# Kernel optimization log

Measured on AMD Instinct MI355X. Metric: run time of the kernel, lower is better.

## Reference

```python
import jax, jax.numpy as jnp
import numpy as np

NEG = -1e9


def setup_inputs() -> dict:
    key = jax.random.key(0)
    ks = jax.random.split(key, 9)
    B, L, S, E = 8, 2048, 2048, 1024
    H, G, KD, VD = 16, 64, 1024, 1024
    return {
        "query": jax.random.normal(ks[0], (B, L, E), jnp.float32),
        "key": jax.random.normal(ks[1], (B, S, E), jnp.float32),
        "value": jax.random.normal(ks[2], (B, S, E), jnp.float32),
        "other": jnp.zeros((1,), jnp.float32),
        "key_padding_mask": jax.random.bernoulli(ks[3], 0.1, (B, S)),
        "nhead": H,
        "query_proj": jax.random.normal(ks[4], (1, E, KD), jnp.float32) * 0.02,
        "key_proj": jax.random.normal(ks[5], (1, E, KD), jnp.float32) * 0.02,
        "value_proj": jax.random.normal(ks[6], (1, E, VD), jnp.float32) * 0.02,
        "importance_proj": jax.random.normal(ks[7], (1, E, H * G), jnp.float32) * 0.02,
        "output_proj": jax.random.normal(ks[8], (1, VD, E), jnp.float32) * 0.02,
    }


def reference(query, key, value, other, key_padding_mask, nhead,
              query_proj, key_proj, value_proj, importance_proj, output_proj):
    B, L, E = query.shape
    S = key.shape[1]
    H = nhead
    KD = query_proj.shape[-1]
    VD = value_proj.shape[-1]
    Ek, Ev = KD // H, VD // H
    G = importance_proj.shape[-1] // H
    scale = 1.0 / jnp.sqrt(jnp.asarray(Ek, query.dtype))

    # projections -> (B, H, L/S, d)
    qs = (query @ query_proj[0]).reshape(B, L, H, Ek).transpose(0, 2, 1, 3)
    kk = (key @ key_proj[0]).reshape(B, S, H, Ek).transpose(0, 2, 1, 3)
    vs = (value @ value_proj[0]).reshape(B, S, H, Ev).transpose(0, 2, 1, 3)

    # importance-weighted global queries: softmax over L
    ips = (query @ importance_proj[0]).reshape(B, L, H, G).transpose(0, 2, 3, 1)  # (B,H,G,L)
    ips = jax.nn.softmax(ips, axis=-1)
    gqs = jnp.einsum('bhgl,bhld->bhgd', ips, qs)  # (B,H,G,Ek)

    # stage 1: global queries attend over all keys (shared attn for keys & values)
    g_scores = jnp.einsum('bhgd,bhsd->bhgs', gqs, kk) * scale  # (B,H,G,S)
    g_scores = jnp.where(key_padding_mask[:, None, None, :], NEG, g_scores)
    g_attn = jax.nn.softmax(g_scores, axis=-1)
    global_keys = jnp.einsum('bhgs,bhsd->bhgd', g_attn, kk)   # (B,H,G,Ek)
    global_values = jnp.einsum('bhgs,bhsd->bhgd', g_attn, vs)  # (B,H,G,Ev)

    # stage 2: local queries attend over G global keys/values
    l_scores = jnp.einsum('bhld,bhgd->bhlg', qs, global_keys) * scale  # (B,H,L,G)
    l_attn = jax.nn.softmax(l_scores, axis=-1)
    out = jnp.einsum('bhlg,bhgd->bhld', l_attn, global_values)  # (B,H,L,Ev)

    out = out.transpose(0, 2, 1, 3).reshape(B, L, H * Ev)
    out = out @ output_proj[0]  # (B,L,E)
    return (out, l_attn)
```

## Files before the change

### kernel.cpp

```cpp
#include <hip/hip_runtime.h>


typedef float f32x4 __attribute__((ext_vector_type(4)));
typedef _Float16 f16x8 __attribute__((ext_vector_type(8)));
typedef unsigned short u16;

#define DEV static __device__ __forceinline__

DEV u16 f2h(float x){
  _Float16 h = (_Float16)x;
  return __builtin_bit_cast(u16, h);
}
DEV float h2f(u16 u){
  return (float)__builtin_bit_cast(_Float16, u);
}
DEV void split1h(float x, u16 &h, u16 &l){
  h = f2h(x);
  l = f2h(x - h2f(h));
}
DEV unsigned pk2h(float a, float b){
  return (unsigned)f2h(a) | ((unsigned)f2h(b) << 16);
}

DEV void gload16(const u16* src, u16* dst_lds){
  __builtin_amdgcn_global_load_lds(
      (__attribute__((address_space(1))) void*)src,
      (__attribute__((address_space(3))) void*)dst_lds, 16, 0, 0);
}

__global__ __launch_bounds__(256)
void mask_norm(const unsigned char* __restrict__ src, unsigned char* __restrict__ dst, int n)
{
  const unsigned* w = (const unsigned*)src;
  const int tid = threadIdx.x;
  int local = 0;
  for (int i = tid; i < n/4; i += 256){
    unsigned v = w[i];
    if (v == 0x3F800000u) local |= 2;
    else if (v > 1u)      local |= 1;
  }
  __shared__ int red[256];
  red[tid] = local;
  __syncthreads();
  for (int s = 128; s; s >>= 1){
    if (tid < s) red[tid] |= red[tid+s];
    __syncthreads();
  }
  const int r = red[0];
  const int mode = (r & 2) ? 2 : ((r & 1) ? 1 : 0);
  for (int i = tid; i < n; i += 256){
    unsigned char v;
    if (mode == 1) v = src[i] ? 1 : 0;
    else           v = w[i]   ? 1 : 0;
    dst[i] = v;
  }
}

__global__ __launch_bounds__(256)
void conv_hi(const float* __restrict__ x, u16* __restrict__ hi, int n8)
{
  const int i = blockIdx.x*256 + threadIdx.x;
  if (i >= n8) return;
  f32x4 a = ((const f32x4*)x)[2*i], b = ((const f32x4*)x)[2*i+1];
  uint4 uh;
  uh.x = pk2h(a[0], a[1]); uh.y = pk2h(a[2], a[3]);
  uh.z = pk2h(b[0], b[1]); uh.w = pk2h(b[2], b[3]);
  ((uint4*)hi)[i] = uh;
}

__global__ __launch_bounds__(256)
void transpose_hi5(const float* __restrict__ s0, const float* __restrict__ s1,
                   const float* __restrict__ s2, const float* __restrict__ s3,
                   const float* __restrict__ s4,
                   u16* __restrict__ d0, u16* __restrict__ d1, u16* __restrict__ d2,
                   u16* __restrict__ d3, u16* __restrict__ d4)
{
  const int z = blockIdx.z;
  const float* Wsrc = z == 0 ? s0 : z == 1 ? s1 : z == 2 ? s2 : z == 3 ? s3 : s4;
  u16* Whi = z == 0 ? d0 : z == 1 ? d1 : z == 2 ? d2 : z == 3 ? d3 : d4;
  __shared__ float t[64][65];
  const int tid = threadIdx.x;
  const int n0 = blockIdx.x * 64, k0 = blockIdx.y * 64;
  #pragma unroll
  for (int it = 0; it < 16; ++it){
    int e = it*256 + tid, r = e >> 6, c = e & 63;
    t[r][c] = Wsrc[(long)(k0+r)*1024 + (n0+c)];
  }
  __syncthreads();
  #pragma unroll
  for (int it = 0; it < 16; ++it){
    int e = it*256 + tid, r = e >> 6, c = e & 63;
    Whi[(long)(n0+r)*1024 + (k0+c)] = f2h(t[c][r]);
  }
}

template<int TM, int TERMS, int CM, int EPI, int SWZ>
__global__ __launch_bounds__(256)
void gemm_g(const u16* __restrict__ Ah_g, const u16* __restrict__ Al_g,
            const u16* __restrict__ Bh_g,
            void* __restrict__ Cp, void* __restrict__ Cp2,
            const unsigned char* __restrict__ maskp,
            int K, int lda, int ldb, int ldc,
            long aB, long aH, long bB, long bH, long cB, long cH,
            int H2, int Ssz, float scale)
{
  constexpr int BN = 128, BK = 32;
  constexpr int WM = TM/2, WN = BN/2;
  constexpr int FM = WM/16, FN = WN/16;
  __shared__ __align__(16) u16 AhS[2][TM*BK];
  __shared__ __align__(16) u16 AlS[2][TERMS == 2 ? TM*BK : 8];
  __shared__ __align__(16) u16 BhS[2][BN*BK];

  const int tid = threadIdx.x;
  int bx = blockIdx.x, by = blockIdx.y;
  if constexpr (SWZ){
    const int gx = gridDim.x;
    const int nwg = gx * gridDim.y;
    const int q = nwg >> 3;
    const int flat = bx + gx * by;
    const int nf = (flat & 7) * q + (flat >> 3);
    bx = nf % gx; by = nf / gx;
  }
  const int batch = blockIdx.z;
  const int b = batch / H2, h = batch - b*H2;
  const long aOff = (long)b*aB + (long)h*aH;
  const long bOff = (long)b*bB + (long)h*bH;
  const long cOff = (long)b*cB + (long)h*cH;
  const int nBase = bx * BN;
  const int mBase = by * TM;
  const int wave = tid >> 6, lane = tid & 63;
  const int wm = wave >> 1, wn = wave & 1;
  const int cg8 = (lane & 3) * 8;
  const int rsub = lane >> 2;

  auto stage = [&](int buf, int k0){
    #pragma unroll
    for (int c = 0; c < TM/64; ++c){
      const int chunk = wave*(TM/64) + c;
      const long g = aOff + (long)(mBase + chunk*16 + rsub)*lda + k0 + cg8;
      gload16(Ah_g + g, &AhS[buf][chunk*512]);
      if constexpr (TERMS == 2) gload16(Al_g + g, &AlS[buf][chunk*512]);
    }
    #pragma unroll
    for (int c = 0; c < 2; ++c){
      const int chunk = wave*2 + c;
      const long g = bOff + (long)(nBase + chunk*16 + rsub)*ldb + k0 + cg8;
      gload16(Bh_g + g, &BhS[buf][chunk*512]);
    }
  };

  f32x4 acc[FM][FN] = {};

  stage(0, 0);
  __syncthreads();
  const int nk = K >> 5;
  for (int t = 0; t < nk; ++t){
    const int buf = t & 1;
    if (t + 1 < nk) stage(buf ^ 1, (t + 1) << 5);

    f16x8 ah[FM], al[FM], bh[FN];
    #pragma unroll
    for (int mi = 0; mi < FM; ++mi){
      const int off = (wm*WM + mi*16 + (lane & 15))*BK + (lane >> 4)*8;
      ah[mi] = *(const f16x8*)&AhS[buf][off];
      if constexpr (TERMS == 2) al[mi] = *(const f16x8*)&AlS[buf][off];
    }
    #pragma unroll
    for (int ni = 0; ni < FN; ++ni){
      const int off = (wn*WN + ni*16 + (lane & 15))*BK + (lane >> 4)*8;
      bh[ni] = *(const f16x8*)&BhS[buf][off];
    }
    #pragma unroll
    for (int mi = 0; mi < FM; ++mi)
      #pragma unroll
      for (int ni = 0; ni < FN; ++ni){
        acc[mi][ni] = __builtin_amdgcn_mfma_f32_16x16x32_f16(ah[mi], bh[ni], acc[mi][ni], 0, 0, 0);
        if constexpr (TERMS == 2)
          acc[mi][ni] = __builtin_amdgcn_mfma_f32_16x16x32_f16(al[mi], bh[ni], acc[mi][ni], 0, 0, 0);
      }
    __syncthreads();
  }

  const int cr = (lane >> 4) * 4, cc = lane & 15;
  #pragma unroll
  for (int mi = 0; mi < FM; ++mi)
    #pragma unroll
    for (int ni = 0; ni < FN; ++ni)
      #pragma unroll
      for (int r = 0; r < 4; ++r){
        const int row = mBase + wm*WM + mi*16 + cr + r;
        const int col = nBase + wn*WN + ni*16 + cc;
        float v = acc[mi][ni][r];
        if constexpr (EPI == 1){
          v *= scale;
          if (maskp[(long)b*Ssz + col]) v = -50000.0f;
        }
        const long ci = cOff + (long)row*ldc + col;
        if constexpr (CM == 0){
          ((float*)Cp)[ci] = v;
        } else {
          u16 hh, ll;
          split1h(v, hh, ll);
          ((u16*)Cp)[ci]  = hh;
          ((u16*)Cp2)[ci] = ll;
        }
      }
}

struct PArg {
  const void* Ap;
  const u16*  Bh;
  u16* Ch; u16* Cl;
  long bB, cB;
  int lda, ldb, ldc;
  int nbx, nby;
};

template<int TM, int AMODE>
__global__ __launch_bounds__(256)
void gemm_pair(PArg a0, PArg a1, int n0, int K)
{
  constexpr int BN = 128, BK = 32;
  constexpr int WM = TM/2, WN = BN/2;
  constexpr int FM = WM/16, FN = WN/16;
  constexpr int NC = TM/64;
  __shared__ __align__(16) u16 AhS[2][TM*BK];
  __shared__ __align__(16) u16 BhS[2][BN*BK];

  const int tid = threadIdx.x;
  const int gid = blockIdx.x;
  const PArg P = (gid < n0) ? a0 : a1;
  int lid = (gid < n0) ? gid : gid - n0;
  const int gsz = (gid < n0) ? n0 : ((int)gridDim.x - n0);
  {
    const int q = gsz >> 3;
    lid = (lid & 7) * q + (lid >> 3);
  }
  const int bx = lid % P.nbx;
  const int rest = lid / P.nbx;
  const int by = rest % P.nby;
  const int z  = rest / P.nby;
  const long bOff = (long)z * P.bB;
  const long cOff = (long)z * P.cB;
  const int nBase = bx * BN;
  const int mBase = by * TM;
  const int wave = tid >> 6, lane = tid & 63;
  const int wm = wave >> 1, wn = wave & 1;
  const int cg8 = (lane & 3) * 8;
  const int rsub = lane >> 2;

  const u16* Au = (const u16*)P.Ap;
  const float* Af = (const float*)P.Ap;

  auto stageB = [&](int buf, int k0){
    #pragma unroll
    for (int c = 0; c < 2; ++c){
      const int chunk = wave*2 + c;
      const long g = bOff + (long)(nBase + chunk*16 + rsub)*P.ldb + k0 + cg8;
      gload16(P.Bh + g, &BhS[buf][chunk*512]);
    }
  };
  auto stageA_g = [&](int buf, int k0){
    #pragma unroll
    for (int c = 0; c < NC; ++c){
      const int chunk = wave*NC + c;
      const long g = (long)(mBase + chunk*16 + rsub)*P.lda + k0 + cg8;
      gload16(Au + g, &AhS[buf][chunk*512]);
    }
  };

  f32x4 acc[FM][FN] = {};
  f32x4 sA0[NC], sA1[NC];

  auto loadA_f = [&](int k0){
    #pragma unroll
    for (int c = 0; c < NC; ++c){
      const int chunk = wave*NC + c;
      const long g = (long)(mBase + chunk*16 + rsub)*P.lda + k0 + cg8;
      sA0[c] = *(const f32x4*)(Af + g);
      sA1[c] = *(const f32x4*)(Af + g + 4);
    }
  };
  auto writeA_f = [&](int buf){
    #pragma unroll
    for (int c = 0; c < NC; ++c){
      const int chunk = wave*NC + c;
      uint4 u;
      u.x = pk2h(sA0[c][0], sA0[c][1]); u.y = pk2h(sA0[c][2], sA0[c][3]);
      u.z = pk2h(sA1[c][0], sA1[c][1]); u.w = pk2h(sA1[c][2], sA1[c][3]);
      *(uint4*)&AhS[buf][chunk*512 + (long)lane*8] = u;
    }
  };

  stageB(0, 0);
  if constexpr (AMODE == 1) stageA_g(0, 0);
  else { loadA_f(0); writeA_f(0); }
  __syncthreads();

  const int nk = K >> 5;
  for (int t = 0; t < nk; ++t){
    const int buf = t & 1;
    if (t + 1 < nk){
      stageB(buf ^ 1, (t + 1) << 5);
      if constexpr (AMODE == 1) stageA_g(buf ^ 1, (t + 1) << 5);
      else loadA_f((t + 1) << 5);
    }

    f16x8 ah[FM], bh[FN];
    #pragma unroll
    for (int mi = 0; mi < FM; ++mi){
      const int off = (wm*WM + mi*16 + (lane & 15))*BK + (lane >> 4)*8;
      ah[mi] = *(const f16x8*)&AhS[buf][off];
    }
    #pragma unroll
    for (int ni = 0; ni < FN; ++ni){
      const int off = (wn*WN + ni*16 + (lane & 15))*BK + (lane >> 4)*8;
      bh[ni] = *(const f16x8*)&BhS[buf][off];
    }
    #pragma unroll
    for (int mi = 0; mi < FM; ++mi)
      #pragma unroll
      for (int ni = 0; ni < FN; ++ni)
        acc[mi][ni] = __builtin_amdgcn_mfma_f32_16x16x32_f16(ah[mi], bh[ni], acc[mi][ni], 0, 0, 0);

    if constexpr (AMODE == 0){
      if (t + 1 < nk) writeA_f(buf ^ 1);
    }
    __syncthreads();
  }

  const int cr = (lane >> 4) * 4, cc = lane & 15;
  #pragma unroll
  for (int mi = 0; mi < FM; ++mi)
    #pragma unroll
    for (int ni = 0; ni < FN; ++ni)
      #pragma unroll
      for (int r = 0; r < 4; ++r){
        const int row = mBase + wm*WM + mi*16 + cr + r;
        const int col = nBase + wn*WN + ni*16 + cc;
        const long ci = cOff + (long)row*P.ldc + col;
        u16 hh, ll;
        split1h(acc[mi][ni][r], hh, ll);
        P.Ch[ci] = hh;
        P.Cl[ci] = ll;
      }
}

template<int NB>
__global__ __launch_bounds__(256)
void flash_agg(const u16* __restrict__ Sh_g, const u16* __restrict__ Sl_g,
               const u16* __restrict__ B1h_g, const u16* __restrict__ B1l_g,
               const u16* __restrict__ B2h_g, const u16* __restrict__ B2l_g,
               float* __restrict__ P1, float* __restrict__ P2,
               float* __restrict__ msm, float* __restrict__ mss,
               int K, int KC, int lda, int ldb,
               long aB, long aH, long bB, long bH, int H2, int nbatch)
{
  __shared__ __align__(16) u16 Ph[64][72], Pl[64][72];
  __shared__ __align__(16) u16 B1hS[64][72], B1lS[64][72];
  __shared__ __align__(16) u16 B2hS[NB==2?64:1][72], B2lS[NB==2?64:1][72];
  __shared__ float mS[64], sS[64], fS[64];
  const int tid = threadIdx.x;
  const int kc = blockIdx.x, batch = blockIdx.y;
  const int b = batch / H2, h = batch - b*H2;
  const long aOff = (long)b*aB + (long)h*aH;
  const long bOff = (long)b*bB + (long)h*bH;
  const int kchunk = K / KC, kbeg = kc * kchunk;
  const int wm = tid >> 6, lane = tid & 63;
  const int srow = tid >> 2, sq = tid & 3;

  if (tid < 64){ mS[tid] = -1e30f; sS[tid] = 0.f; }

  f32x4 acc1[4] = {}, acc2[4] = {};

  for (int ks = kbeg; ks < kbeg + kchunk; ks += 64){
    __syncthreads();
    #pragma unroll
    for (int it = 0; it < 4; ++it){
      const int e = it*256 + tid;
      const int lr = e >> 4, d0 = (e & 15) * 4;
      const long gm = bOff + (long)(ks + lr)*ldb + d0;
      ushort4 h4 = *(const ushort4*)(B1h_g + gm);
      ushort4 l4 = *(const ushort4*)(B1l_g + gm);
      B1hS[d0+0][lr]=h4.x; B1hS[d0+1][lr]=h4.y; B1hS[d0+2][lr]=h4.z; B1hS[d0+3][lr]=h4.w;
      B1lS[d0+0][lr]=l4.x; B1lS[d0+1][lr]=l4.y; B1lS[d0+2][lr]=l4.z; B1lS[d0+3][lr]=l4.w;
      if constexpr (NB == 2){
        ushort4 h42 = *(const ushort4*)(B2h_g + gm);
        ushort4 l42 = *(const ushort4*)(B2l_g + gm);
        B2hS[d0+0][lr]=h42.x; B2hS[d0+1][lr]=h42.y; B2hS[d0+2][lr]=h42.z; B2hS[d0+3][lr]=h42.w;
        B2lS[d0+0][lr]=l42.x; B2lS[d0+1][lr]=l42.y; B2lS[d0+2][lr]=l42.z; B2lS[d0+3][lr]=l42.w;
      }
    }

    float v[16];
    {
      const long ga = aOff + (long)srow*lda + ks + sq*16;
      uint4 ha = *(const uint4*)(Sh_g + ga);
      uint4 hb = *(const uint4*)(Sh_g + ga + 8);
      uint4 la = *(const uint4*)(Sl_g + ga);
      uint4 lb = *(const uint4*)(Sl_g + ga + 8);
      v[0]=h2f((u16)ha.x)+h2f((u16)la.x);  v[1]=h2f((u16)(ha.x>>16))+h2f((u16)(la.x>>16));
      v[2]=h2f((u16)ha.y)+h2f((u16)la.y);  v[3]=h2f((u16)(ha.y>>16))+h2f((u16)(la.y>>16));
      v[4]=h2f((u16)ha.z)+h2f((u16)la.z);  v[5]=h2f((u16)(ha.z>>16))+h2f((u16)(la.z>>16));
      v[6]=h2f((u16)ha.w)+h2f((u16)la.w);  v[7]=h2f((u16)(ha.w>>16))+h2f((u16)(la.w>>16));
      v[8]=h2f((u16)hb.x)+h2f((u16)lb.x);  v[9]=h2f((u16)(hb.x>>16))+h2f((u16)(lb.x>>16));
      v[10]=h2f((u16)hb.y)+h2f((u16)lb.y); v[11]=h2f((u16)(hb.y>>16))+h2f((u16)(lb.y>>16));
      v[12]=h2f((u16)hb.z)+h2f((u16)lb.z); v[13]=h2f((u16)(hb.z>>16))+h2f((u16)(lb.z>>16));
      v[14]=h2f((u16)hb.w)+h2f((u16)lb.w); v[15]=h2f((u16)(hb.w>>16))+h2f((u16)(lb.w>>16));
    }
    float mx = v[0];
    #pragma unroll
    for (int i = 1; i < 16; ++i) mx = fmaxf(mx, v[i]);
    mx = fmaxf(mx, __shfl_xor(mx, 1));
    mx = fmaxf(mx, __shfl_xor(mx, 2));
    const float mold = mS[srow];
    const float mnew = fmaxf(mold, mx);
    float sum = 0.f;
    u16 ph[16], pl[16];
    #pragma unroll
    for (int i = 0; i < 16; ++i){
      float e = __expf(v[i] - mnew);
      sum += e;
      split1h(e, ph[i], pl[i]);
    }
    sum += __shfl_xor(sum, 1);
    sum += __shfl_xor(sum, 2);
    if (sq == 0){
      const float f = __expf(mold - mnew);
      sS[srow] = sS[srow] * f + sum;
      mS[srow] = mnew;
      fS[srow] = f;
    }
    {
      uint4 uh0, uh1, ul0, ul1;
      uh0.x=(unsigned)ph[0]|((unsigned)ph[1]<<16);  uh0.y=(unsigned)ph[2]|((unsigned)ph[3]<<16);
      uh0.z=(unsigned)ph[4]|((unsigned)ph[5]<<16);  uh0.w=(unsigned)ph[6]|((unsigned)ph[7]<<16);
      uh1.x=(unsigned)ph[8]|((unsigned)ph[9]<<16);  uh1.y=(unsigned)ph[10]|((unsigned)ph[11]<<16);
      uh1.z=(unsigned)ph[12]|((unsigned)ph[13]<<16);uh1.w=(unsigned)ph[14]|((unsigned)ph[15]<<16);
      ul0.x=(unsigned)pl[0]|((unsigned)pl[1]<<16);  ul0.y=(unsigned)pl[2]|((unsigned)pl[3]<<16);
      ul0.z=(unsigned)pl[4]|((unsigned)pl[5]<<16);  ul0.w=(unsigned)pl[6]|((unsigned)pl[7]<<16);
      ul1.x=(unsigned)pl[8]|((unsigned)pl[9]<<16);  ul1.y=(unsigned)pl[10]|((unsigned)pl[11]<<16);
      ul1.z=(unsigned)pl[12]|((unsigned)pl[13]<<16);ul1.w=(unsigned)pl[14]|((unsigned)pl[15]<<16);
      *(uint4*)&Ph[srow][sq*16]     = uh0;
      *(uint4*)&Ph[srow][sq*16 + 8] = uh1;
      *(uint4*)&Pl[srow][sq*16]     = ul0;
      *(uint4*)&Pl[srow][sq*16 + 8] = ul1;
    }
    __syncthreads();

    float fr4[4];
    #pragma unroll
    for (int r = 0; r < 4; ++r) fr4[r] = fS[wm*16 + (lane >> 4)*4 + r];
    #pragma unroll
    for (int ni = 0; ni < 4; ++ni)
      #pragma unroll
      for (int r = 0; r < 4; ++r){
        acc1[ni][r] *= fr4[r];
        if constexpr (NB == 2) acc2[ni][r] *= fr4[r];
      }
    #pragma unroll
    for (int k0 = 0; k0 < 64; k0 += 32){
      const int ko = k0 + (lane >> 4)*8;
      const int fr = lane & 15;
      f16x8 a_h = *(const f16x8*)&Ph[wm*16 + fr][ko];
      f16x8 a_l = *(const f16x8*)&Pl[wm*16 + fr][ko];
      #pragma unroll
      for (int ni = 0; ni < 4; ++ni){
        f16x8 b_h = *(const f16x8*)&B1hS[ni*16 + fr][ko];
        f16x8 b_l = *(const f16x8*)&B1lS[ni*16 + fr][ko];
        acc1[ni] = __builtin_amdgcn_mfma_f32_16x16x32_f16(a_h, b_h, acc1[ni], 0, 0, 0);
        acc1[ni] = __builtin_amdgcn_mfma_f32_16x16x32_f16(a_l, b_h, acc1[ni], 0, 0, 0);
        acc1[ni] = __builtin_amdgcn_mfma_f32_16x16x32_f16(a_h, b_l, acc1[ni], 0, 0, 0);
        if constexpr (NB == 2){
          f16x8 c_h = *(const f16x8*)&B2hS[ni*16 + fr][ko];
          f16x8 c_l = *(const f16x8*)&B2lS[ni*16 + fr][ko];
          acc2[ni] = __builtin_amdgcn_mfma_f32_16x16x32_f16(a_h, c_h, acc2[ni], 0, 0, 0);
          acc2[ni] = __builtin_amdgcn_mfma_f32_16x16x32_f16(a_l, c_h, acc2[ni], 0, 0, 0);
          acc2[ni] = __builtin_amdgcn_mfma_f32_16x16x32_f16(a_h, c_l, acc2[ni], 0, 0, 0);
        }
      }
    }
  }

  const long po = ((long)(kc*nbatch + batch) << 12);
  const int cr = (lane >> 4) * 4, cc = lane & 15;
  #pragma unroll
  for (int ni = 0; ni < 4; ++ni)
    #pragma unroll
    for (int r = 0; r < 4; ++r){
      const int g = wm*16 + cr + r, d = ni*16 + cc;
      P1[po + g*64 + d] = acc1[ni][r];
      if constexpr (NB == 2) P2[po + g*64 + d] = acc2[ni][r];
    }
  if (tid < 64){
    msm[((long)kc*nbatch + batch)*64 + tid] = mS[tid];
    mss[((long)kc*nbatch + batch)*64 + tid] = sS[tid];
  }
}

template<int NB, int KC>
__global__ __launch_bounds__(256)
void flash_combine(const float* __restrict__ P1, const float* __restrict__ P2,
                   const float* __restrict__ msm, const float* __restrict__ mss,
                   u16* __restrict__ o1h, u16* __restrict__ o1l,
                   u16* __restrict__ o2h, u16* __restrict__ o2l, int nbatch)
{
  const int batch = blockIdx.x;
  const int tid = threadIdx.x;
  const int g = tid >> 2, dq = (tid & 3) * 16;
  float m[KC], s[KC], w[KC];
  float M = -1e30f;
  #pragma unroll
  for (int c = 0; c < KC; ++c){
    m[c] = msm[((long)c*nbatch + batch)*64 + g];
    s[c] = mss[((long)c*nbatch + batch)*64 + g];
    M = fmaxf(M, m[c]);
  }
  float den = 0.f;
  #pragma unroll
  for (int c = 0; c < KC; ++c){ w[c] = __expf(m[c] - M); den += s[c]*w[c]; }
  const float inv = 1.0f / den;
  #pragma unroll
  for (int c = 0; c < KC; ++c) w[c] *= inv;
  const long oo = (long)batch*4096 + g*64 + dq;
  #pragma unroll
  for (int nb = 0; nb < NB; ++nb){
    const float* Pa = nb ? P2 : P1;
    u16* oh = nb ? o2h : o1h;
    u16* ol = nb ? o2l : o1l;
    u16 hh[16], ll[16];
    #pragma unroll
    for (int j = 0; j < 4; ++j){
      f32x4 a = {0.f, 0.f, 0.f, 0.f};
      #pragma unroll
      for (int c = 0; c < KC; ++c){
        f32x4 p = *(const f32x4*)(Pa + (((long)c*nbatch + batch) << 12) + g*64 + dq + j*4);
        a += p * w[c];
      }
      #pragma unroll
      for (int e = 0; e < 4; ++e) split1h(a[e], hh[j*4+e], ll[j*4+e]);
    }
    uint4 uh0, uh1, ul0, ul1;
    uh0.x=(unsigned)hh[0]|((unsigned)hh[1]<<16);  uh0.y=(unsigned)hh[2]|((unsigned)hh[3]<<16);
    uh0.z=(unsigned)hh[4]|((unsigned)hh[5]<<16);  uh0.w=(unsigned)hh[6]|((unsigned)hh[7]<<16);
    uh1.x=(unsigned)hh[8]|((unsigned)hh[9]<<16);  uh1.y=(unsigned)hh[10]|((unsigned)hh[11]<<16);
    uh1.z=(unsigned)hh[12]|((unsigned)hh[13]<<16);uh1.w=(unsigned)hh[14]|((unsigned)hh[15]<<16);
    ul0.x=(unsigned)ll[0]|((unsigned)ll[1]<<16);  ul0.y=(unsigned)ll[2]|((unsigned)ll[3]<<16);
    ul0.z=(unsigned)ll[4]|((unsigned)ll[5]<<16);  ul0.w=(unsigned)ll[6]|((unsigned)ll[7]<<16);
    ul1.x=(unsigned)ll[8]|((unsigned)ll[9]<<16);  ul1.y=(unsigned)ll[10]|((unsigned)ll[11]<<16);
    ul1.z=(unsigned)ll[12]|((unsigned)ll[13]<<16);ul1.w=(unsigned)ll[14]|((unsigned)ll[15]<<16);
    *(uint4*)(oh + oo)     = uh0;
    *(uint4*)(oh + oo + 8) = uh1;
    *(uint4*)(ol + oo)     = ul0;
    *(uint4*)(ol + oo + 8) = ul1;
  }
}

__global__ __launch_bounds__(256)
void stage2_mfma(const u16* __restrict__ qhi, const u16* __restrict__ qlo,
                 const u16* __restrict__ gkh_g, const u16* __restrict__ gkl_g,
                 const u16* __restrict__ gvh_g, const u16* __restrict__ gvl_g,
                 float* __restrict__ lattn, u16* __restrict__ ahi,
                 float scale)
{
  __shared__ __align__(16) u16 Ah[128][72];
  __shared__ __align__(16) u16 Al[128][72];
  __shared__ __align__(16) u16 Bh[64][72];
  __shared__ __align__(16) u16 Bl[64][72];
  const int tid = threadIdx.x;
  const int bh = blockIdx.y;
  const int b = bh >> 4, h = bh & 15;
  const int l0 = blockIdx.x * 128;
  const int wm = tid >> 6, lane = tid & 63;

  const long qbase = ((long)b*2048 + l0)*1024 + h*64;
  #pragma unroll
  for (int it = 0; it < 4; ++it){
    const int e = it*256 + tid, row = e >> 3, s = e & 7;
    const long g = qbase + (long)row*1024 + s*8;
    *(uint4*)&Ah[row][s*8] = *(const uint4*)(qhi + g);
    *(uint4*)&Al[row][s*8] = *(const uint4*)(qlo + g);
  }
  const long gb = (long)bh * 4096;
  #pragma unroll
  for (int it = 0; it < 2; ++it){
    const int e = it*256 + tid, gr = e >> 3, s = e & 7;
    *(uint4*)&Bh[gr][s*8] = *(const uint4*)(gkh_g + gb + gr*64 + s*8);
    *(uint4*)&Bl[gr][s*8] = *(const uint4*)(gkl_g + gb + gr*64 + s*8);
  }
  __syncthreads();

  f32x4 acc[2][4] = {};
  #pragma unroll
  for (int k0 = 0; k0 < 64; k0 += 32){
    f16x8 a_h[2], a_l[2], b_h[4], b_l[4];
    #pragma unroll
    for (int mi = 0; mi < 2; ++mi){
      const int row = wm*32 + mi*16 + (lane & 15);
      a_h[mi] = *(const f16x8*)&Ah[row][k0 + (lane >> 4)*8];
      a_l[mi] = *(const f16x8*)&Al[row][k0 + (lane >> 4)*8];
    }
    #pragma unroll
    for (int ni = 0; ni < 4; ++ni){
      const int nr = ni*16 + (lane & 15);
      b_h[ni] = *(const f16x8*)&Bh[nr][k0 + (lane >> 4)*8];
      b_l[ni] = *(const f16x8*)&Bl[nr][k0 + (lane >> 4)*8];
    }
    #pragma unroll
    for (int mi = 0; mi < 2; ++mi)
      #pragma unroll
      for (int ni = 0; ni < 4; ++ni){
        acc[mi][ni] = __builtin_amdgcn_mfma_f32_16x16x32_f16(a_h[mi], b_h[ni], acc[mi][ni], 0, 0, 0);
        acc[mi][ni] = __builtin_amdgcn_mfma_f32_16x16x32_f16(a_l[mi], b_h[ni], acc[mi][ni], 0, 0, 0);
        acc[mi][ni] = __builtin_amdgcn_mfma_f32_16x16x32_f16(a_h[mi], b_l[ni], acc[mi][ni], 0, 0, 0);
      }
  }
  __syncthreads();

  #pragma unroll
  for (int it = 0; it < 4; ++it){
    const int e = it*256 + tid;
    const int gr = e >> 4, d0 = (e & 15) * 4;
    ushort4 vh = *(const ushort4*)(gvh_g + gb + gr*64 + d0);
    ushort4 vl = *(const ushort4*)(gvl_g + gb + gr*64 + d0);
    Bh[d0+0][gr] = vh.x; Bh[d0+1][gr] = vh.y; Bh[d0+2][gr] = vh.z; Bh[d0+3][gr] = vh.w;
    Bl[d0+0][gr] = vl.x; Bl[d0+1][gr] = vl.y; Bl[d0+2][gr] = vl.z; Bl[d0+3][gr] = vl.w;
  }

  #pragma unroll
  for (int mi = 0; mi < 2; ++mi){
    #pragma unroll
    for (int r = 0; r < 4; ++r){
      float v0 = acc[mi][0][r]*scale, v1 = acc[mi][1][r]*scale;
      float v2 = acc[mi][2][r]*scale, v3 = acc[mi][3][r]*scale;
      float mx = fmaxf(fmaxf(v0,v1), fmaxf(v2,v3));
      #pragma unroll
      for (int off = 1; off < 16; off <<= 1) mx = fmaxf(mx, __shfl_xor(mx, off, 16));
      float e0 = __expf(v0-mx), e1 = __expf(v1-mx), e2 = __expf(v2-mx), e3 = __expf(v3-mx);
      float sum = (e0+e1) + (e2+e3);
      #pragma unroll
      for (int off = 1; off < 16; off <<= 1) sum += __shfl_xor(sum, off, 16);
      const float inv = 1.0f / sum;
      e0 *= inv; e1 *= inv; e2 *= inv; e3 *= inv;
      const int lrow = wm*32 + mi*16 + (lane >> 4)*4 + r;
      float* lp = lattn + ((long)bh*2048 + l0 + lrow)*64 + (lane & 15);
      lp[0] = e0; lp[16] = e1; lp[32] = e2; lp[48] = e3;
      u16 hh, ll;
      split1h(e0, hh, ll); Ah[lrow][ 0 + (lane&15)] = hh; Al[lrow][ 0 + (lane&15)] = ll;
      split1h(e1, hh, ll); Ah[lrow][16 + (lane&15)] = hh; Al[lrow][16 + (lane&15)] = ll;
      split1h(e2, hh, ll); Ah[lrow][32 + (lane&15)] = hh; Al[lrow][32 + (lane&15)] = ll;
      split1h(e3, hh, ll); Ah[lrow][48 + (lane&15)] = hh; Al[lrow][48 + (lane&15)] = ll;
    }
  }
  __syncthreads();

  f32x4 o[2][4] = {};
  #pragma unroll
  for (int k0 = 0; k0 < 64; k0 += 32){
    f16x8 p_h[2], p_l[2], b_h[4], b_l[4];
    #pragma unroll
    for (int mi = 0; mi < 2; ++mi){
      const int row = wm*32 + mi*16 + (lane & 15);
      p_h[mi] = *(const f16x8*)&Ah[row][k0 + (lane >> 4)*8];
      p_l[mi] = *(const f16x8*)&Al[row][k0 + (lane >> 4)*8];
    }
    #pragma unroll
    for (int ni = 0; ni < 4; ++ni){
      const int nr = ni*16 + (lane & 15);
      b_h[ni] = *(const f16x8*)&Bh[nr][k0 + (lane >> 4)*8];
      b_l[ni] = *(const f16x8*)&Bl[nr][k0 + (lane >> 4)*8];
    }
    #pragma unroll
    for (int mi = 0; mi < 2; ++mi)
      #pragma unroll
      for (int ni = 0; ni < 4; ++ni){
        o[mi][ni] = __builtin_amdgcn_mfma_f32_16x16x32_f16(p_h[mi], b_h[ni], o[mi][ni], 0, 0, 0);
        o[mi][ni] = __builtin_amdgcn_mfma_f32_16x16x32_f16(p_l[mi], b_h[ni], o[mi][ni], 0, 0, 0);
        o[mi][ni] = __builtin_amdgcn_mfma_f32_16x16x32_f16(p_h[mi], b_l[ni], o[mi][ni], 0, 0, 0);
      }
  }

  #pragma unroll
  for (int mi = 0; mi < 2; ++mi)
    #pragma unroll
    for (int ni = 0; ni < 4; ++ni)
      #pragma unroll
      for (int r = 0; r < 4; ++r){
        const int lrow = wm*32 + mi*16 + (lane >> 4)*4 + r;
        const int d = ni*16 + (lane & 15);
        const long oidx = ((long)b*2048 + l0 + lrow)*1024 + h*64 + d;
        ahi[oidx] = f2h(o[mi][ni][r]);
      }
}

extern "C" void kernel_launch(void* const* d_in, const int* in_sizes, int n_in,
                              void* d_out, int out_size, void* d_ws, size_t ws_size,
                              hipStream_t stream)
{
  const float* query = (const float*)d_in[0];
  const float* key   = (const float*)d_in[1];
  const float* value = (const float*)d_in[2];
  const unsigned char* mask_raw = (const unsigned char*)d_in[4];
  const float* Wq = (const float*)d_in[6];
  const float* Wk = (const float*)d_in[7];
  const float* Wv = (const float*)d_in[8];
  const float* Wi = (const float*)d_in[9];
  const float* Wo = (const float*)d_in[10];
  float* out0 = (float*)d_out;
  float* out1 = out0 + 16777216;

  char* ws = (char*)d_ws;
  u16* WoT_hi = (u16*)(ws + 0);
  float* msm_q = (float*)(ws + (2L<<20));
  float* mss_q = (float*)(ws + (2L<<20) + 262144);
  float* msm_g = (float*)(ws + (3L<<20));
  float* mss_g = (float*)(ws + (3L<<20) + 262144);
  u16* WqT_hi = (u16*)(ws + (4L<<20));
  unsigned char* mask_ws = (unsigned char*)(ws + (6L<<20));
  float* part1 = (float*)(ws + (4L<<20));
  u16* WkT_hi = (u16*)(ws + (8L<<20));
  u16* WvT_hi = (u16*)(ws + (12L<<20));
  float* part2 = (float*)(ws + (12L<<20));
  u16* gqs_hi = (u16*)(ws + (16L<<20));
  u16* gqs_lo = (u16*)(ws + (17L<<20));
  u16* WiT_hi = (u16*)(ws + (18L<<20));
  u16* qp_hi  = (u16*)(ws + (20L<<20));
  u16* gsc_hi = (u16*)(ws + (20L<<20));
  u16* gsc_lo = (u16*)(ws + (52L<<20));
  u16* qs_hi  = (u16*)(ws + (84L<<20));
  u16* qs_lo  = (u16*)(ws + (116L<<20));
  float* partg = (float*)(ws + (148L<<20));
  u16* vs_hi  = (u16*)(ws + (148L<<20));
  u16* vs_lo  = (u16*)(ws + (180L<<20));
  u16* ips_hi = (u16*)(ws + (212L<<20));
  u16* ips_lo = (u16*)(ws + (244L<<20));
  u16* kk_hi  = (u16*)(ws + (212L<<20));
  u16* kk_lo  = (u16*)(ws + (244L<<20));
  u16* gk_hi  = (u16*)(ws + (212L<<20));
  u16* gk_lo  = (u16*)(ws + (213L<<20));
  u16* gv_hi  = (u16*)(ws + (214L<<20));
  u16* gv_lo  = (u16*)(ws + (215L<<20));
  u16* attn_hi = (u16*)(ws + (244L<<20));

  const dim3 blk(256);
  const float scale = 0.125f;

  mask_norm<<<1, blk, 0, stream>>>(mask_raw, mask_ws, 16384);
  transpose_hi5<<<dim3(16,16,5), blk, 0, stream>>>(Wq, Wk, Wv, Wi, Wo,
      WqT_hi, WkT_hi, WvT_hi, WiT_hi, WoT_hi);
  conv_hi<<<8192, blk, 0, stream>>>(query, qp_hi, 2097152);

  {
    PArg g0 = { qp_hi,  WqT_hi, qs_hi,  qs_lo,  0L, 0L,
                1024, 1024, 1024, 8, 128 };
    PArg g1 = { WiT_hi, qp_hi,  ips_hi, ips_lo, 2097152L, 2097152L,
                1024, 1024, 2048, 16, 8 };
    gemm_pair<128,1><<<2048, blk, 0, stream>>>(g0, g1, 1024, 1024);
  }

  flash_agg<1><<<dim3(4,128), blk, 0, stream>>>(
      ips_hi, ips_lo, qs_hi, qs_lo, nullptr, nullptr,
      partg, nullptr, msm_q, mss_q,
      2048, 4, 2048, 1024, 2097152L, 131072L, 2097152L, 64L, 16, 128);
  flash_combine<1,4><<<128, blk, 0, stream>>>(
      partg, nullptr, msm_q, mss_q, gqs_hi, gqs_lo, nullptr, nullptr, 128);

  {
    PArg g0 = { key,   WkT_hi, kk_hi, kk_lo, 0L, 0L, 1024, 1024, 1024, 8, 128 };
    PArg g1 = { value, WvT_hi, vs_hi, vs_lo, 0L, 0L, 1024, 1024, 1024, 8, 128 };
    gemm_pair<128,0><<<2048, blk, 0, stream>>>(g0, g1, 1024, 1024);
  }

  gemm_g<64,2,1,1,0><<<dim3(16,1,128), blk, 0, stream>>>(
      gqs_hi, gqs_lo, kk_hi, gsc_hi, gsc_lo, mask_ws,
      64, 64,1024,2048, 65536L,4096L, 2097152L,64L, 2097152L,131072L, 16, 2048, scale);

  flash_agg<2><<<dim3(4,128), blk, 0, stream>>>(
      gsc_hi, gsc_lo, kk_hi, kk_lo, vs_hi, vs_lo,
      part1, part2, msm_g, mss_g,
      2048, 4, 2048, 1024, 2097152L, 131072L, 2097152L, 64L, 16, 128);
  flash_combine<2,4><<<128, blk, 0, stream>>>(
      part1, part2, msm_g, mss_g, gk_hi, gk_lo, gv_hi, gv_lo, 128);

  stage2_mfma<<<dim3(16,128), blk, 0, stream>>>(qs_hi, qs_lo, gk_hi, gk_lo,
      gv_hi, gv_lo, out1, attn_hi, scale);

  gemm_g<128,1,0,0,1><<<dim3(8,128,1), blk, 0, stream>>>(
      attn_hi, nullptr, WoT_hi, out0, nullptr, nullptr,
      1024, 1024,1024,1024, 0,0, 0,0, 0,0, 1, 2048, 1.f);

  (void)in_sizes; (void)n_in; (void)out_size; (void)ws_size;
}
```

Before: 517.0 us.

## Fuse key/value projection GEMM with global-query flash aggregation in one launch

Adds a combined kernel that runs the key/value projection GEMMs (now converting fp32 input to fp16 on the fly in a new device GEMM) and the importance-weighted flash aggregation for global queries as independent blocks of a single grid. Doubles the K-split for both flash aggregation stages from 4 to 8 so each has 1024 blocks, and moves partial buffers to a fresh workspace region to avoid aliasing. The intent is to fill the GPU with independent work and remove the tail of the small 512-block flash launches, at the cost of extra partial-combine traffic and a GEMM path without the previous pre-converted A operand.

```diff
diff --git a/kernel.cpp b/kernel.cpp
--- a/kernel.cpp
+++ b/kernel.cpp
@@ -346,22 +346,125 @@
       }
 }
 
-template<int NB>
-__global__ __launch_bounds__(256)
-void flash_agg(const u16* __restrict__ Sh_g, const u16* __restrict__ Sl_g,
-               const u16* __restrict__ B1h_g, const u16* __restrict__ B1l_g,
-               const u16* __restrict__ B2h_g, const u16* __restrict__ B2l_g,
-               float* __restrict__ P1, float* __restrict__ P2,
-               float* __restrict__ msm, float* __restrict__ mss,
-               int K, int KC, int lda, int ldb,
-               long aB, long aH, long bB, long bH, int H2, int nbatch)
-{
-  __shared__ __align__(16) u16 Ph[64][72], Pl[64][72];
-  __shared__ __align__(16) u16 B1hS[64][72], B1lS[64][72];
-  __shared__ __align__(16) u16 B2hS[NB==2?64:1][72], B2lS[NB==2?64:1][72];
-  __shared__ float mS[64], sS[64], fS[64];
-  const int tid = threadIdx.x;
-  const int kc = blockIdx.x, batch = blockIdx.y;
+DEV void dev_gemm_f32A(const PArg P, int lid, int tid, char* sm, int K)
+{
+  constexpr int BK = 32;
+  constexpr int FM = 4, FN = 4, NC = 2;
+  u16* AhS = (u16*)sm;
+  u16* BhS = (u16*)(sm + 16384);
+
+  const int bx = lid % P.nbx;
+  const int rest = lid / P.nbx;
+  const int by = rest % P.nby;
+  const int z  = rest / P.nby;
+  const long bOff = (long)z * P.bB;
+  const long cOff = (long)z * P.cB;
+  const int nBase = bx * 128;
+  const int mBase = by * 128;
+  const int wave = tid >> 6, lane = tid & 63;
+  const int wm = wave >> 1, wn = wave & 1;
+  const int cg8 = (lane & 3) * 8;
+  const int rsub = lane >> 2;
+
+  const float* Af = (const float*)P.Ap;
+
+  auto stageB = [&](int buf, int k0){
+    #pragma unroll
+    for (int c = 0; c < 2; ++c){
+      const int chunk = wave*2 + c;
+      const long g = bOff + (long)(nBase + chunk*16 + rsub)*P.ldb + k0 + cg8;
+      gload16(P.Bh + g, &BhS[buf*4096 + chunk*512]);
+    }
+  };
+
+  f32x4 acc[FM][FN] = {};
+  f32x4 sA0[NC], sA1[NC];
+
+  auto loadA_f = [&](int k0){
+    #pragma unroll
+    for (int c = 0; c < NC; ++c){
+      const int chunk = wave*NC + c;
+      const long g = (long)(mBase + chunk*16 + rsub)*P.lda + k0 + cg8;
+      sA0[c] = *(const f32x4*)(Af + g);
+      sA1[c] = *(const f32x4*)(Af + g + 4);
+    }
+  };
+  auto writeA_f = [&](int buf){
+    #pragma unroll
+    for (int c = 0; c < NC; ++c){
+      const int chunk = wave*NC + c;
+      uint4 u;
+      u.x = pk2h(sA0[c][0], sA0[c][1]); u.y = pk2h(sA0[c][2], sA0[c][3]);
+      u.z = pk2h(sA1[c][0], sA1[c][1]); u.w = pk2h(sA1[c][2], sA1[c][3]);
+      *(uint4*)&AhS[buf*4096 + chunk*512 + lane*8] = u;
+    }
+  };
+
+  stageB(0, 0);
+  loadA_f(0); writeA_f(0);
+  __syncthreads();
+
+  const int nk = K >> 5;
+  for (int t = 0; t < nk; ++t){
+    const int buf = t & 1;
+    if (t + 1 < nk){
+      stageB(buf ^ 1, (t + 1) << 5);
+      loadA_f((t + 1) << 5);
+    }
+
+    f16x8 ah[FM], bh[FN];
+    #pragma unroll
+    for (int mi = 0; mi < FM; ++mi){
+      const int off = (wm*64 + mi*16 + (lane & 15))*BK + (lane >> 4)*8;
+      ah[mi] = *(const f16x8*)&AhS[buf*4096 + off];
+    }
+    #pragma unroll
+    for (int ni = 0; ni < FN; ++ni){
+      const int off = (wn*64 + ni*16 + (lane & 15))*BK + (lane >> 4)*8;
+      bh[ni] = *(const f16x8*)&BhS[buf*4096 + off];
+    }
+    #pragma unroll
+    for (int mi = 0; mi < FM; ++mi)
+      #pragma unroll
+      for (int ni = 0; ni < FN; ++ni)
+        acc[mi][ni] = __builtin_amdgcn_mfma_f32_16x16x32_f16(ah[mi], bh[ni], acc[mi][ni], 0, 0, 0);
+
+    if (t + 1 < nk) writeA_f(buf ^ 1);
+    __syncthreads();
+  }
+
+  const int cr = (lane >> 4) * 4, cc = lane & 15;
+  #pragma unroll
+  for (int mi = 0; mi < FM; ++mi)
+    #pragma unroll
+    for (int ni = 0; ni < FN; ++ni)
+      #pragma unroll
+      for (int r = 0; r < 4; ++r){
+        const int row = mBase + wm*64 + mi*16 + cr + r;
+        const int col = nBase + wn*64 + ni*16 + cc;
+        const long ci = cOff + (long)row*P.ldc + col;
+        u16 hh, ll;
+        split1h(acc[mi][ni][r], hh, ll);
+        P.Ch[ci] = hh;
+        P.Cl[ci] = ll;
+      }
+}
+
+DEV void dev_flash1(const u16* Sh_g, const u16* Sl_g,
+                    const u16* B1h_g, const u16* B1l_g,
+                    float* P1, float* msm, float* mss,
+                    int kc, int batch, int tid, char* sm,
+                    int K, int KC, int lda, int ldb,
+                    long aB, long aH, long bB, long bH, int H2, int nbatch)
+{
+  u16 (*Ph)[72]   = (u16(*)[72])(sm);
+  u16 (*Pl)[72]   = (u16(*)[72])(sm + 9216);
+  u16 (*B1hS)[72] = (u16(*)[72])(sm + 18432);
+  u16 (*B1lS)[72] = (u16(*)[72])(sm + 27648);
+  float* mS = (float*)(sm + 36864);
+  float* sS = (float*)(sm + 37120);
+  float* fS = (float*)(sm + 37376);
+
   const int b = batch / H2, h = batch - b*H2;
   const long aOff = (long)b*aB + (long)h*aH;
   const long bOff = (long)b*bB + (long)h*bH;
@@ -371,7 +474,7 @@
 
   if (tid < 64){ mS[tid] = -1e30f; sS[tid] = 0.f; }
 
-  f32x4 acc1[4] = {}, acc2[4] = {};
+  f32x4 acc1[4] = {};
 
   for (int ks = kbeg; ks < kbeg + kchunk; ks += 64){
     __syncthreads();
@@ -384,12 +487,6 @@
       ushort4 l4 = *(const ushort4*)(B1l_g + gm);
       B1hS[d0+0][lr]=h4.x; B1hS[d0+1][lr]=h4.y; B1hS[d0+2][lr]=h4.z; B1hS[d0+3][lr]=h4.w;
       B1lS[d0+0][lr]=l4.x; B1lS[d0+1][lr]=l4.y; B1lS[d0+2][lr]=l4.z; B1lS[d0+3][lr]=l4.w;
-      if constexpr (NB == 2){
-        ushort4 h42 = *(const ushort4*)(B2h_g + gm);
-        ushort4 l42 = *(const ushort4*)(B2l_g + gm);
-        B2hS[d0+0][lr]=h42.x; B2hS[d0+1][lr]=h42.y; B2hS[d0+2][lr]=h42.z; B2hS[d0+3][lr]=h42.w;
-        B2lS[d0+0][lr]=l42.x; B2lS[d0+1][lr]=l42.y; B2lS[d0+2][lr]=l42.z; B2lS[d0+3][lr]=l42.w;
-      }
     }
 
     float v[16];
@@ -454,6 +551,169 @@
     #pragma unroll
     for (int ni = 0; ni < 4; ++ni)
       #pragma unroll
+      for (int r = 0; r < 4; ++r)
+        acc1[ni][r] *= fr4[r];
+    #pragma unroll
+    for (int k0 = 0; k0 < 64; k0 += 32){
+      const int ko = k0 + (lane >> 4)*8;
+      const int fr = lane & 15;
+      f16x8 a_h = *(const f16x8*)&Ph[wm*16 + fr][ko];
+      f16x8 a_l = *(const f16x8*)&Pl[wm*16 + fr][ko];
+      #pragma unroll
+      for (int ni = 0; ni < 4; ++ni){
+        f16x8 b_h = *(const f16x8*)&B1hS[ni*16 + fr][ko];
+        f16x8 b_l = *(const f16x8*)&B1lS[ni*16 + fr][ko];
+        acc1[ni] = __builtin_amdgcn_mfma_f32_16x16x32_f16(a_h, b_h, acc1[ni], 0, 0, 0);
+        acc1[ni] = __builtin_amdgcn_mfma_f32_16x16x32_f16(a_l, b_h, acc1[ni], 0, 0, 0);
+        acc1[ni] = __builtin_amdgcn_mfma_f32_16x16x32_f16(a_h, b_l, acc1[ni], 0, 0, 0);
+      }
+    }
+  }
+
+  const long po = ((long)(kc*nbatch + batch) << 12);
+  const int cr = (lane >> 4) * 4, cc = lane & 15;
+  #pragma unroll
+  for (int ni = 0; ni < 4; ++ni)
+    #pragma unroll
+    for (int r = 0; r < 4; ++r){
+      const int g = wm*16 + cr + r, d = ni*16 + cc;
+      P1[po + g*64 + d] = acc1[ni][r];
+    }
+  if (tid < 64){
+    msm[((long)kc*nbatch + batch)*64 + tid] = mS[tid];
+    mss[((long)kc*nbatch + batch)*64 + tid] = sS[tid];
+  }
+}
+
+__global__ __launch_bounds__(256)
+void pair_flash(PArg a0, PArg a1,
+                const u16* Sh, const u16* Sl, const u16* B1h, const u16* B1l,
+                float* P1, float* msm, float* mss, int K)
+{
+  extern __shared__ char smdyn[];
+  const int gid = blockIdx.x;
+  const int tid = threadIdx.x;
+  if (gid < 2048){
+    const PArg P = (gid < 1024) ? a0 : a1;
+    int lid = (gid < 1024) ? gid : gid - 1024;
+    lid = (lid & 7) * 128 + (lid >> 3);
+    dev_gemm_f32A(P, lid, tid, smdyn, K);
+  } else {
+    const int l2 = gid - 2048;
+    dev_flash1(Sh, Sl, B1h, B1l, P1, msm, mss,
+               l2 >> 7, l2 & 127, tid, smdyn,
+               2048, 8, 2048, 1024, 2097152L, 131072L, 2097152L, 64L, 16, 128);
+  }
+}
+
+template<int NB>
+__global__ __launch_bounds__(256)
+void flash_agg(const u16* __restrict__ Sh_g, const u16* __restrict__ Sl_g,
+               const u16* __restrict__ B1h_g, const u16* __restrict__ B1l_g,
+               const u16* __restrict__ B2h_g, const u16* __restrict__ B2l_g,
+               float* __restrict__ P1, float* __restrict__ P2,
+               float* __restrict__ msm, float* __restrict__ mss,
+               int K, int KC, int lda, int ldb,
+               long aB, long aH, long bB, long bH, int H2, int nbatch)
+{
+  __shared__ __align__(16) u16 Ph[64][72], Pl[64][72];
+  __shared__ __align__(16) u16 B1hS[64][72], B1lS[64][72];
+  __shared__ __align__(16) u16 B2hS[NB==2?64:1][72], B2lS[NB==2?64:1][72];
+  __shared__ float mS[64], sS[64], fS[64];
+  const int tid = threadIdx.x;
+  const int kc = blockIdx.x, batch = blockIdx.y;
+  const int b = batch / H2, h = batch - b*H2;
+  const long aOff = (long)b*aB + (long)h*aH;
+  const long bOff = (long)b*bB + (long)h*bH;
+  const int kchunk = K / KC, kbeg = kc * kchunk;
+  const int wm = tid >> 6, lane = tid & 63;
+  const int srow = tid >> 2, sq = tid & 3;
+
+  if (tid < 64){ mS[tid] = -1e30f; sS[tid] = 0.f; }
+
+  f32x4 acc1[4] = {}, acc2[4] = {};
+
+  for (int ks = kbeg; ks < kbeg + kchunk; ks += 64){
+    __syncthreads();
+    #pragma unroll
+    for (int it = 0; it < 4; ++it){
+      const int e = it*256 + tid;
+      const int lr = e >> 4, d0 = (e & 15) * 4;
+      const long gm = bOff + (long)(ks + lr)*ldb + d0;
+      ushort4 h4 = *(const ushort4*)(B1h_g + gm);
+      ushort4 l4 = *(const ushort4*)(B1l_g + gm);
+      B1hS[d0+0][lr]=h4.x; B1hS[d0+1][lr]=h4.y; B1hS[d0+2][lr]=h4.z; B1hS[d0+3][lr]=h4.w;
+      B1lS[d0+0][lr]=l4.x; B1lS[d0+1][lr]=l4.y; B1lS[d0+2][lr]=l4.z; B1lS[d0+3][lr]=l4.w;
+      if constexpr (NB == 2){
+        ushort4 h42 = *(const ushort4*)(B2h_g + gm);
+        ushort4 l42 = *(const ushort4*)(B2l_g + gm);
+        B2hS[d0+0][lr]=h42.x; B2hS[d0+1][lr]=h42.y; B2hS[d0+2][lr]=h42.z; B2hS[d0+3][lr]=h42.w;
+        B2lS[d0+0][lr]=l42.x; B2lS[d0+1][lr]=l42.y; B2lS[d0+2][lr]=l42.z; B2lS[d0+3][lr]=l42.w;
+      }
+    }
+
+    float v[16];
+    {
+      const long ga = aOff + (long)srow*lda + ks + sq*16;
+      uint4 ha = *(const uint4*)(Sh_g + ga);
+      uint4 hb = *(const uint4*)(Sh_g + ga + 8);
+      uint4 la = *(const uint4*)(Sl_g + ga);
+      uint4 lb = *(const uint4*)(Sl_g + ga + 8);
+      v[0]=h2f((u16)ha.x)+h2f((u16)la.x);  v[1]=h2f((u16)(ha.x>>16))+h2f((u16)(la.x>>16));
+      v[2]=h2f((u16)ha.y)+h2f((u16)la.y);  v[3]=h2f((u16)(ha.y>>16))+h2f((u16)(la.y>>16));
+      v[4]=h2f((u16)ha.z)+h2f((u16)la.z);  v[5]=h2f((u16)(ha.z>>16))+h2f((u16)(la.z>>16));
+      v[6]=h2f((u16)ha.w)+h2f((u16)la.w);  v[7]=h2f((u16)(ha.w>>16))+h2f((u16)(la.w>>16));
+      v[8]=h2f((u16)hb.x)+h2f((u16)lb.x);  v[9]=h2f((u16)(hb.x>>16))+h2f((u16)(lb.x>>16));
+      v[10]=h2f((u16)hb.y)+h2f((u16)lb.y); v[11]=h2f((u16)(hb.y>>16))+h2f((u16)(lb.y>>16));
+      v[12]=h2f((u16)hb.z)+h2f((u16)lb.z); v[13]=h2f((u16)(hb.z>>16))+h2f((u16)(lb.z>>16));
+      v[14]=h2f((u16)hb.w)+h2f((u16)lb.w); v[15]=h2f((u16)(hb.w>>16))+h2f((u16)(lb.w>>16));
+    }
+    float mx = v[0];
+    #pragma unroll
+    for (int i = 1; i < 16; ++i) mx = fmaxf(mx, v[i]);
+    mx = fmaxf(mx, __shfl_xor(mx, 1));
+    mx = fmaxf(mx, __shfl_xor(mx, 2));
+    const float mold = mS[srow];
+    const float mnew = fmaxf(mold, mx);
+    float sum = 0.f;
+    u16 ph[16], pl[16];
+    #pragma unroll
+    for (int i = 0; i < 16; ++i){
+      float e = __expf(v[i] - mnew);
+      sum += e;
+      split1h(e, ph[i], pl[i]);
+    }
+    sum += __shfl_xor(sum, 1);
+    sum += __shfl_xor(sum, 2);
+    if (sq == 0){
+      const float f = __expf(mold - mnew);
+      sS[srow] = sS[srow] * f + sum;
+      mS[srow] = mnew;
+      fS[srow] = f;
+    }
+    {
+      uint4 uh0, uh1, ul0, ul1;
+      uh0.x=(unsigned)ph[0]|((unsigned)ph[1]<<16);  uh0.y=(unsigned)ph[2]|((unsigned)ph[3]<<16);
+      uh0.z=(unsigned)ph[4]|((unsigned)ph[5]<<16);  uh0.w=(unsigned)ph[6]|((unsigned)ph[7]<<16);
+      uh1.x=(unsigned)ph[8]|((unsigned)ph[9]<<16);  uh1.y=(unsigned)ph[10]|((unsigned)ph[11]<<16);
+      uh1.z=(unsigned)ph[12]|((unsigned)ph[13]<<16);uh1.w=(unsigned)ph[14]|((unsigned)ph[15]<<16);
+      ul0.x=(unsigned)pl[0]|((unsigned)pl[1]<<16);  ul0.y=(unsigned)pl[2]|((unsigned)pl[3]<<16);
+      ul0.z=(unsigned)pl[4]|((unsigned)pl[5]<<16);  ul0.w=(unsigned)pl[6]|((unsigned)pl[7]<<16);
+      ul1.x=(unsigned)pl[8]|((unsigned)pl[9]<<16);  ul1.y=(unsigned)pl[10]|((unsigned)pl[11]<<16);
+      ul1.z=(unsigned)pl[12]|((unsigned)pl[13]<<16);ul1.w=(unsigned)pl[14]|((unsigned)pl[15]<<16);
+      *(uint4*)&Ph[srow][sq*16]     = uh0;
+      *(uint4*)&Ph[srow][sq*16 + 8] = uh1;
+      *(uint4*)&Pl[srow][sq*16]     = ul0;
+      *(uint4*)&Pl[srow][sq*16 + 8] = ul1;
+    }
+    __syncthreads();
+
+    float fr4[4];
+    #pragma unroll
+    for (int r = 0; r < 4; ++r) fr4[r] = fS[wm*16 + (lane >> 4)*4 + r];
+    #pragma unroll
+    for (int ni = 0; ni < 4; ++ni)
+      #pragma unroll
       for (int r = 0; r < 4; ++r){
         acc1[ni][r] *= fr4[r];
         if constexpr (NB == 2) acc2[ni][r] *= fr4[r];
@@ -717,10 +977,8 @@
   float* mss_g = (float*)(ws + (3L<<20) + 262144);
   u16* WqT_hi = (u16*)(ws + (4L<<20));
   unsigned char* mask_ws = (unsigned char*)(ws + (6L<<20));
-  float* part1 = (float*)(ws + (4L<<20));
   u16* WkT_hi = (u16*)(ws + (8L<<20));
   u16* WvT_hi = (u16*)(ws + (12L<<20));
-  float* part2 = (float*)(ws + (12L<<20));
   u16* gqs_hi = (u16*)(ws + (16L<<20));
   u16* gqs_lo = (u16*)(ws + (17L<<20));
   u16* WiT_hi = (u16*)(ws + (18L<<20));
@@ -729,7 +987,6 @@
   u16* gsc_lo = (u16*)(ws + (52L<<20));
   u16* qs_hi  = (u16*)(ws + (84L<<20));
   u16* qs_lo  = (u16*)(ws + (116L<<20));
-  float* partg = (float*)(ws + (148L<<20));
   u16* vs_hi  = (u16*)(ws + (148L<<20));
   u16* vs_lo  = (u16*)(ws + (180L<<20));
   u16* ips_hi = (u16*)(ws + (212L<<20));
@@ -741,6 +998,9 @@
   u16* gv_hi  = (u16*)(ws + (214L<<20));
   u16* gv_lo  = (u16*)(ws + (215L<<20));
   u16* attn_hi = (u16*)(ws + (244L<<20));
+  float* partg = (float*)(ws + (280L<<20));
+  float* part1 = (float*)(ws + (280L<<20));
+  float* part2 = (float*)(ws + (300L<<20));
 
   const dim3 blk(256);
   const float scale = 0.125f;
@@ -758,28 +1018,24 @@
     gemm_pair<128,1><<<2048, blk, 0, stream>>>(g0, g1, 1024, 1024);
   }
 
-  flash_agg<1><<<dim3(4,128), blk, 0, stream>>>(
-      ips_hi, ips_lo, qs_hi, qs_lo, nullptr, nullptr,
-      partg, nullptr, msm_q, mss_q,
-      2048, 4, 2048, 1024, 2097152L, 131072L, 2097152L, 64L, 16, 128);
-  flash_combine<1,4><<<128, blk, 0, stream>>>(
-      partg, nullptr, msm_q, mss_q, gqs_hi, gqs_lo, nullptr, nullptr, 128);
-
   {
     PArg g0 = { key,   WkT_hi, kk_hi, kk_lo, 0L, 0L, 1024, 1024, 1024, 8, 128 };
     PArg g1 = { value, WvT_hi, vs_hi, vs_lo, 0L, 0L, 1024, 1024, 1024, 8, 128 };
-    gemm_pair<128,0><<<2048, blk, 0, stream>>>(g0, g1, 1024, 1024);
-  }
+    pair_flash<<<3072, blk, 37632, stream>>>(g0, g1,
+        ips_hi, ips_lo, qs_hi, qs_lo, partg, msm_q, mss_q, 1024);
+  }
+  flash_combine<1,8><<<128, blk, 0, stream>>>(
+      partg, nullptr, msm_q, mss_q, gqs_hi, gqs_lo, nullptr, nullptr, 128);
 
   gemm_g<64,2,1,1,0><<<dim3(16,1,128), blk, 0, stream>>>(
       gqs_hi, gqs_lo, kk_hi, gsc_hi, gsc_lo, mask_ws,
       64, 64,1024,2048, 65536L,4096L, 2097152L,64L, 2097152L,131072L, 16, 2048, scale);
 
-  flash_agg<2><<<dim3(4,128), blk, 0, stream>>>(
+  flash_agg<2><<<dim3(8,128), blk, 0, stream>>>(
       gsc_hi, gsc_lo, kk_hi, kk_lo, vs_hi, vs_lo,
       part1, part2, msm_g, mss_g,
-      2048, 4, 2048, 1024, 2097152L, 131072L, 2097152L, 64L, 16, 128);
-  flash_combine<2,4><<<128, blk, 0, stream>>>(
+      2048, 8, 2048, 1024, 2097152L, 131072L, 2097152L, 64L, 16, 128);
+  flash_combine<2,8><<<128, blk, 0, stream>>>(
       part1, part2, msm_g, mss_g, gk_hi, gk_lo, gv_hi, gv_lo, 128);
 
   stage2_mfma<<<dim3(16,128), blk, 0, stream>>>(qs_hi, qs_lo, gk_hi, gk_lo,
```

New measurement: 511.3 us. No clear change (-1.1%).
